# Kernel optimization log

Measured on AMD Instinct MI355X. Metric: run time of the kernel, lower is better.

## Reference

```python
import jax, jax.numpy as jnp
import numpy as np

N, D, K = 131072, 64, 4096


def setup_inputs() -> dict:
    key = jax.random.key(0)
    k1, k2 = jax.random.split(key)
    x = jax.random.normal(k1, (N, D), dtype=jnp.float32)
    embed = jax.random.normal(k2, (K, D), dtype=jnp.float32)
    return {"x": x, "embed": embed}


def reference(x, embed):
    """EuclideanCodebook forward.

    x:     [N, D] flat input vectors
    embed: [K, D] codebook
    Returns (quantize [N,D], embed_ind [N], cluster_size [K], embed_sum [K,D]).
    cluster_size / embed_sum are the one-hot scatter statistics fed to the
    EMA codebook update (embed_onehot.sum(0) and flatten^T @ embed_onehot).
    """
    num_codes = embed.shape[0]
    x2 = jnp.sum(x * x, axis=-1, keepdims=True)               # [N, 1]
    e2 = jnp.sum(embed * embed, axis=-1)                      # [K]
    dist = x2 - 2.0 * (x @ embed.T) + e2[None, :]             # [N, K]
    embed_ind = jnp.argmin(dist, axis=-1)                     # [N]
    quantize = embed[embed_ind]                               # gather [N, D]
    # scatter statistics for EMA update
    cluster_size = jnp.zeros((num_codes,), x.dtype).at[embed_ind].add(1.0)  # [K]
    embed_sum = jax.ops.segment_sum(x, embed_ind, num_segments=num_codes)   # [K, D]
    return quantize, embed_ind, cluster_size, embed_sum
```

## Files before the change

### kernel.cpp

```cpp
#include <hip/hip_runtime.h>

#define N_ROWS 131072
#define DIM 64
#define K_CODES 4096
#define BROWS 128
#define CK 64
#define NCH (K_CODES / CK)
#define EST 72
#define EPS 0.015625f
#define HEPS 0.0078125f

typedef __attribute__((ext_vector_type(8))) short short8;
typedef __attribute__((ext_vector_type(4))) float f32x4;

__device__ inline unsigned short bf16rn(float f) {
    unsigned int u = __float_as_uint(f);
    u += 0x7FFFu + ((u >> 16) & 1u);
    return (unsigned short)(u >> 16);
}
__device__ inline unsigned int fkey(float f) {
    unsigned int u = __float_as_uint(f);
    return (u & 0x80000000u) ? ~u : (u | 0x80000000u);
}

__global__ void pack_kernel(const float* __restrict__ embed,
                            unsigned short* __restrict__ ebf,
                            float* __restrict__ e2,
                            float* __restrict__ e2h,
                            int* __restrict__ cnt,
                            float* __restrict__ cs) {
    const int g = blockIdx.x * blockDim.x + threadIdx.x;
    for (int i = g; i < K_CODES + K_CODES * DIM; i += K_CODES * 16)
        cs[i] = 0.f;
    if (g == 0) *cnt = 0;

    const int code = g >> 4;
    const int w    = g & 15;
    const int half = w >> 3;
    const int d0   = (w & 7) << 3;
    const float* ep = embed + (size_t)code * DIM + d0;
    float4 f0 = *(const float4*)ep;
    float4 f1 = *(const float4*)(ep + 4);
    float wv[8] = {f0.x, f0.y, f0.z, f0.w, f1.x, f1.y, f1.z, f1.w};
    unsigned short o[8];
    float ssq = 0.f;
#pragma unroll
    for (int j = 0; j < 8; ++j) {
        unsigned short hb = bf16rn(wv[j]);
        if (half == 0) {
            o[j] = hb;
            ssq = fmaf(wv[j], wv[j], ssq);
        } else {
            float hf = __uint_as_float(((unsigned int)hb) << 16);
            o[j] = bf16rn(wv[j] - hf);
        }
    }
    *(uint4*)(ebf + (size_t)code * 128 + half * 64 + d0) = *(uint4*)o;
    ssq += __shfl_xor(ssq, 1, 64);
    ssq += __shfl_xor(ssq, 2, 64);
    ssq += __shfl_xor(ssq, 4, 64);
    if (w == 0) {
        e2[code]  = ssq;
        e2h[code] = -0.5f * ssq;
    }
}

__global__ __launch_bounds__(256, 4) void dist_argmin_kernel(
        const float* __restrict__ x, const unsigned short* __restrict__ ebf,
        const float* __restrict__ e2h, const float* __restrict__ embed,
        int* __restrict__ ind_ws, float* __restrict__ ind_out,
        int* __restrict__ cnt, int* __restrict__ list,
        float* __restrict__ quant, float* __restrict__ cs,
        float* __restrict__ esum, int fused) {
    __shared__ unsigned short esh[2][CK * EST];
    __shared__ unsigned short esl[2][CK * EST];
    __shared__ float e2s[2][CK];

    const int tid  = threadIdx.x;
    const int l15  = tid & 15;
    const int quad = (tid >> 4) & 3;
    const int wave = tid >> 6;
    const int r0w  = blockIdx.x * BROWS + wave * 32;

    const int col = tid >> 2;
    const int dq  = (tid & 3) * 16;

    uint4 sh0, sh1, sl0, sl1;
    float se2 = 0.f;
    {
        const unsigned short* pp = ebf + (size_t)col * 128 + dq;
        sh0 = *(const uint4*)pp;
        sh1 = *(const uint4*)(pp + 8);
        sl0 = *(const uint4*)(pp + 64);
        sl1 = *(const uint4*)(pp + 72);
        if (tid < CK) se2 = e2h[tid];
    }

    short8 ah[2][2], al[2][2];
#pragma unroll
    for (int i = 0; i < 2; ++i)
#pragma unroll
        for (int s = 0; s < 2; ++s) {
            const float* xp = x + (size_t)(r0w + 16 * i + l15) * DIM + 32 * s + 8 * quad;
            float4 f0 = *(const float4*)xp;
            float4 f1 = *(const float4*)(xp + 4);
            float w[8] = {f0.x, f0.y, f0.z, f0.w, f1.x, f1.y, f1.z, f1.w};
            short8 h, l;
#pragma unroll
            for (int j = 0; j < 8; ++j) {
                unsigned short hb = bf16rn(w[j]);
                float hf = __uint_as_float(((unsigned int)hb) << 16);
                h[j] = (short)hb;
                l[j] = (short)bf16rn(w[j] - hf);
            }
            ah[i][s] = h;
            al[i][s] = l;
        }

    *(uint4*)(&esh[0][col * EST + dq])     = sh0;
    *(uint4*)(&esh[0][col * EST + dq + 8]) = sh1;
    *(uint4*)(&esl[0][col * EST + dq])     = sl0;
    *(uint4*)(&esl[0][col * EST + dq + 8]) = sl1;
    if (tid < CK) e2s[0][tid] = se2;

    float s1[8], s2[8];
    int c1[8];
#pragma unroll
    for (int t = 0; t < 8; ++t) { s1[t] = -3.4e38f; s2[t] = -3.4e38f; c1[t] = 0; }

    __syncthreads();

    int cur = 0;
    for (int ch = 0; ch < NCH; ++ch) {
        {
            const int c0n = ((ch + 1) & (NCH - 1)) * CK;
            const unsigned short* pp = ebf + (size_t)(c0n + col) * 128 + dq;
            sh0 = *(const uint4*)pp;
            sh1 = *(const uint4*)(pp + 8);
            sl0 = *(const uint4*)(pp + 64);
            sl1 = *(const uint4*)(pp + 72);
            if (tid < CK) se2 = e2h[c0n + tid];
        }

        const int c0 = ch * CK;

        f32x4 acc[2][4];
#pragma unroll
        for (int j = 0; j < 4; ++j) {
            const float ev = e2s[cur][16 * j + l15];
            const f32x4 iv = {ev, ev, ev, ev};
            acc[0][j] = iv;
            acc[1][j] = iv;
        }

#pragma unroll
        for (int j = 0; j < 4; ++j) {
            const int cb = (16 * j + l15) * EST + 8 * quad;
            short8 bh0 = *(const short8*)(&esh[cur][cb]);
            short8 bh1 = *(const short8*)(&esh[cur][cb + 32]);
            short8 bl0 = *(const short8*)(&esl[cur][cb]);
            short8 bl1 = *(const short8*)(&esl[cur][cb + 32]);
#pragma unroll
            for (int i = 0; i < 2; ++i) {
                f32x4 a = acc[i][j];
                a = __builtin_amdgcn_mfma_f32_16x16x32_bf16(ah[i][0], bh0, a, 0, 0, 0);
                a = __builtin_amdgcn_mfma_f32_16x16x32_bf16(ah[i][1], bh1, a, 0, 0, 0);
                a = __builtin_amdgcn_mfma_f32_16x16x32_bf16(ah[i][0], bl0, a, 0, 0, 0);
                a = __builtin_amdgcn_mfma_f32_16x16x32_bf16(ah[i][1], bl1, a, 0, 0, 0);
                a = __builtin_amdgcn_mfma_f32_16x16x32_bf16(al[i][0], bh0, a, 0, 0, 0);
                a = __builtin_amdgcn_mfma_f32_16x16x32_bf16(al[i][1], bh1, a, 0, 0, 0);
                acc[i][j] = a;
            }
        }

#pragma unroll
        for (int j = 0; j < 4; ++j) {
            const int c = c0 + 16 * j + l15;
#pragma unroll
            for (int i = 0; i < 2; ++i)
#pragma unroll
                for (int r = 0; r < 4; ++r) {
                    float d = acc[i][j][r];
                    const int st = i * 4 + r;
                    bool gt = d > s1[st];
                    s2[st] = fmaxf(fminf(d, s1[st]), s2[st]);
                    c1[st] = gt ? c : c1[st];
                    s1[st] = fmaxf(s1[st], d);
                }
        }

        const int nxt = cur ^ 1;
        *(uint4*)(&esh[nxt][col * EST + dq])     = sh0;
        *(uint4*)(&esh[nxt][col * EST + dq + 8]) = sh1;
        *(uint4*)(&esl[nxt][col * EST + dq])     = sl0;
        *(uint4*)(&esl[nxt][col * EST + dq + 8]) = sl1;
        if (tid < CK) e2s[nxt][tid] = se2;

        __syncthreads();
        cur = nxt;
    }

#pragma unroll
    for (int st = 0; st < 8; ++st) {
#pragma unroll
        for (int m = 1; m < 16; m <<= 1) {
            float os1 = __shfl_xor(s1[st], m, 64);
            float os2 = __shfl_xor(s2[st], m, 64);
            int   oc1 = __shfl_xor(c1[st], m, 64);
            bool take = (os1 > s1[st]) || (os1 == s1[st] && oc1 < c1[st]);
            float loser = take ? s1[st] : os1;
            s2[st] = fmaxf(fmaxf(s2[st], os2), loser);
            if (take) { s1[st] = os1; c1[st] = oc1; }
        }
    }
    if (l15 == 0) {
#pragma unroll
        for (int st = 0; st < 8; ++st) {
            const int i = st >> 2, r = st & 3;
            const int row = r0w + 16 * i + 4 * quad + r;
            ind_ws[row] = c1[st];
            ind_out[row] = (float)c1[st];
            if (s1[st] - s2[st] < HEPS) {
                int p = atomicAdd(cnt, 1);
                list[p] = row;
            }
        }
    }

    if (fused) {
        int* li = (int*)&esh[0][0];
        if (l15 == 0) {
#pragma unroll
            for (int st = 0; st < 8; ++st) {
                const int i = st >> 2, r = st & 3;
                li[(wave << 5) + 16 * i + 4 * quad + r] = c1[st];
            }
        }
        const int lane = tid & 63;
        for (int t = 0; t < 32; ++t) {
            const int k = li[(wave << 5) + t];
            const size_t row = (size_t)(r0w + t);
            quant[row * DIM + lane] = embed[(size_t)k * DIM + lane];
            float xv = x[row * DIM + lane];
            atomicAdd(&esum[(size_t)k * DIM + lane], xv);
            if (lane == 0) atomicAdd(&cs[k], 1.0f);
        }
    }
}

__global__ void refine_kernel(const float* __restrict__ x,
                              const float* __restrict__ embed,
                              const float* __restrict__ e2g,
                              const int* __restrict__ cnt,
                              const int* __restrict__ list,
                              int* __restrict__ ind_ws,
                              float* __restrict__ ind_out,
                              float* __restrict__ quant,
                              float* __restrict__ cs,
                              float* __restrict__ esum, int fused) {
    __shared__ float xr[DIM];
    __shared__ unsigned long long red[256];
    const int tid = threadIdx.x;
    const int n = *cnt;
    for (int f = blockIdx.x; f < n; f += gridDim.x) {
        const int row = list[f];
        __syncthreads();
        if (tid < 16)
            ((float4*)xr)[tid] = ((const float4*)(x + (size_t)row * DIM))[tid];
        __syncthreads();
        unsigned long long best = ~0ull;
        for (int c = tid; c < K_CODES; c += 256) {
            const float4* ep = (const float4*)(embed + (size_t)c * DIM);
            float d0 = 0.f, d1 = 0.f, d2 = 0.f, d3 = 0.f;
#pragma unroll
            for (int q = 0; q < 16; ++q) {
                float4 ev = ep[q];
                d0 = fmaf(xr[4 * q + 0], ev.x, d0);
                d1 = fmaf(xr[4 * q + 1], ev.y, d1);
                d2 = fmaf(xr[4 * q + 2], ev.z, d2);
                d3 = fmaf(xr[4 * q + 3], ev.w, d3);
            }
            float sc = fmaf(-2.f, (d0 + d1) + (d2 + d3), e2g[c]);
            unsigned long long key =
                ((unsigned long long)fkey(sc) << 32) | (unsigned int)c;
            if (key < best) best = key;
        }
        red[tid] = best;
        __syncthreads();
        for (int w = 128; w > 0; w >>= 1) {
            if (tid < w && red[tid + w] < red[tid]) red[tid] = red[tid + w];
            __syncthreads();
        }
        const int k_new = (int)(red[0] & 0xFFFFFFFFull);
        if (fused) {
            const int k_old = ind_ws[row];
            if (k_new != k_old) {
                if (tid < DIM) {
                    float xv = xr[tid];
                    atomicAdd(&esum[(size_t)k_old * DIM + tid], -xv);
                    atomicAdd(&esum[(size_t)k_new * DIM + tid],  xv);
                    quant[(size_t)row * DIM + tid] =
                        embed[(size_t)k_new * DIM + tid];
                }
                if (tid == 0) {
                    atomicAdd(&cs[k_old], -1.f);
                    atomicAdd(&cs[k_new],  1.f);
                    ind_ws[row] = k_new;
                    ind_out[row] = (float)k_new;
                }
            }
        } else if (tid == 0) {
            ind_ws[row] = k_new;
            ind_out[row] = (float)k_new;
        }
    }
}

__global__ void scatter_kernel(const float* __restrict__ x,
                               const float* __restrict__ embed,
                               const int* __restrict__ ind,
                               float* __restrict__ quant,
                               float* __restrict__ cs,
                               float* __restrict__ esum) {
    const int t = blockIdx.x * blockDim.x + threadIdx.x;
    const int row = t >> 6;
    const int d = t & 63;
    const int k = ind[row];
    quant[t] = embed[(size_t)k * DIM + d];
    atomicAdd(&esum[(size_t)k * DIM + d], x[t]);
    if (d == 0) atomicAdd(&cs[k], 1.0f);
}

extern "C" void kernel_launch(void* const* d_in, const int* in_sizes, int n_in,
                              void* d_out, int out_size, void* d_ws, size_t ws_size,
                              hipStream_t stream) {
    const float* x     = (const float*)d_in[0];
    const float* embed = (const float*)d_in[1];

    float* out     = (float*)d_out;
    float* quant   = out;
    float* ind_out = out + (size_t)N_ROWS * DIM;
    float* cs      = ind_out + N_ROWS;
    float* esum    = cs + K_CODES;

    float* e2   = (float*)d_ws;
    int* cnt    = (int*)(e2 + K_CODES);
    int* list   = cnt + 4;
    int* ind_ws = list + N_ROWS;
    float* e2h  = (float*)(ind_ws + N_ROWS);
    unsigned short* ebf_ws = (unsigned short*)(e2h + K_CODES);
    const size_t ws_need =
        (size_t)((char*)(ebf_ws + (size_t)K_CODES * 128) - (char*)d_ws);

    const int fused = (ws_size >= ws_need) ? 1 : 0;
    unsigned short* ebf = fused ? ebf_ws : (unsigned short*)quant;

    pack_kernel<<<(K_CODES * 16) / 256, 256, 0, stream>>>(
        embed, ebf, e2, e2h, cnt, cs);
    dist_argmin_kernel<<<N_ROWS / BROWS, 256, 0, stream>>>(
        x, ebf, e2h, embed, ind_ws, ind_out, cnt, list, quant, cs, esum, fused);
    refine_kernel<<<512, 256, 0, stream>>>(
        x, embed, e2, cnt, list, ind_ws, ind_out, quant, cs, esum, fused);
    if (!fused)
        scatter_kernel<<<(size_t)N_ROWS * DIM / 256, 256, 0, stream>>>(
            x, embed, ind_ws, quant, cs, esum);
}
```

Baseline: 421.2 us.

## Refine one row per wavefront with shuffle argmin instead of block reduction

The refine kernel now handles four flagged rows per block, one per 64-lane wavefront, each lane scanning a strided subset of codes. The argmin reduction uses wavefront shuffles instead of a shared-memory tree with eight block barriers. This removes most synchronisation per row and makes fuller use of each block. In exchange each lane scans 64 codes serially, and the non-fused path now writes the index only when it changed.

```diff
diff --git a/kernel.cpp b/kernel.cpp
--- a/kernel.cpp
+++ b/kernel.cpp
@@ -248,71 +248,73 @@
     }
 }
 
-__global__ void refine_kernel(const float* __restrict__ x,
-                              const float* __restrict__ embed,
-                              const float* __restrict__ e2g,
-                              const int* __restrict__ cnt,
-                              const int* __restrict__ list,
-                              int* __restrict__ ind_ws,
-                              float* __restrict__ ind_out,
-                              float* __restrict__ quant,
-                              float* __restrict__ cs,
-                              float* __restrict__ esum, int fused) {
-    __shared__ float xr[DIM];
-    __shared__ unsigned long long red[256];
-    const int tid = threadIdx.x;
+__global__ __launch_bounds__(256) void refine_kernel(
+        const float* __restrict__ x,
+        const float* __restrict__ embed,
+        const float* __restrict__ e2g,
+        const int* __restrict__ cnt,
+        const int* __restrict__ list,
+        int* __restrict__ ind_ws,
+        float* __restrict__ ind_out,
+        float* __restrict__ quant,
+        float* __restrict__ cs,
+        float* __restrict__ esum, int fused) {
+    __shared__ float xr[4][DIM];
+    const int tid  = threadIdx.x;
+    const int w    = tid >> 6;
+    const int lane = tid & 63;
     const int n = *cnt;
-    for (int f = blockIdx.x; f < n; f += gridDim.x) {
-        const int row = list[f];
-        __syncthreads();
-        if (tid < 16)
-            ((float4*)xr)[tid] = ((const float4*)(x + (size_t)row * DIM))[tid];
+    for (int f0 = blockIdx.x * 4; f0 < n; f0 += gridDim.x * 4) {
+        const int fi  = f0 + w;
+        const bool act = fi < n;
+        const int row = act ? list[fi] : list[n - 1];
+        xr[w][lane] = x[(size_t)row * DIM + lane];
         __syncthreads();
         unsigned long long best = ~0ull;
-        for (int c = tid; c < K_CODES; c += 256) {
+        for (int p = 0; p < K_CODES / 64; ++p) {
+            const int c = (p << 6) + lane;
             const float4* ep = (const float4*)(embed + (size_t)c * DIM);
             float d0 = 0.f, d1 = 0.f, d2 = 0.f, d3 = 0.f;
-#pragma unroll
+#pragma unroll 4
             for (int q = 0; q < 16; ++q) {
                 float4 ev = ep[q];
-                d0 = fmaf(xr[4 * q + 0], ev.x, d0);
-                d1 = fmaf(xr[4 * q + 1], ev.y, d1);
-                d2 = fmaf(xr[4 * q + 2], ev.z, d2);
-                d3 = fmaf(xr[4 * q + 3], ev.w, d3);
+                d0 = fmaf(xr[w][4 * q + 0], ev.x, d0);
+                d1 = fmaf(xr[w][4 * q + 1], ev.y, d1);
+                d2 = fmaf(xr[w][4 * q + 2], ev.z, d2);
+                d3 = fmaf(xr[w][4 * q + 3], ev.w, d3);
             }
             float sc = fmaf(-2.f, (d0 + d1) + (d2 + d3), e2g[c]);
             unsigned long long key =
                 ((unsigned long long)fkey(sc) << 32) | (unsigned int)c;
-            if (key < best) best = key;
-        }
-        red[tid] = best;
-        __syncthreads();
-        for (int w = 128; w > 0; w >>= 1) {
-            if (tid < w && red[tid + w] < red[tid]) red[tid] = red[tid + w];
-            __syncthreads();
-        }
-        const int k_new = (int)(red[0] & 0xFFFFFFFFull);
-        if (fused) {
+            best = key < best ? key : best;
+        }
+#pragma unroll
+        for (int m = 32; m > 0; m >>= 1) {
+            unsigned long long o = __shfl_xor(best, m, 64);
+            best = o < best ? o : best;
+        }
+        if (act) {
+            const int k_new = (int)(best & 0xFFFFFFFFull);
             const int k_old = ind_ws[row];
             if (k_new != k_old) {
-                if (tid < DIM) {
-                    float xv = xr[tid];
-                    atomicAdd(&esum[(size_t)k_old * DIM + tid], -xv);
-                    atomicAdd(&esum[(size_t)k_new * DIM + tid],  xv);
-                    quant[(size_t)row * DIM + tid] =
-                        embed[(size_t)k_new * DIM + tid];
+                if (fused) {
+                    float xv = xr[w][lane];
+                    atomicAdd(&esum[(size_t)k_old * DIM + lane], -xv);
+                    atomicAdd(&esum[(size_t)k_new * DIM + lane],  xv);
+                    quant[(size_t)row * DIM + lane] =
+                        embed[(size_t)k_new * DIM + lane];
+                    if (lane == 0) {
+                        atomicAdd(&cs[k_old], -1.f);
+                        atomicAdd(&cs[k_new],  1.f);
+                    }
                 }
-                if (tid == 0) {
-                    atomicAdd(&cs[k_old], -1.f);
-                    atomicAdd(&cs[k_new],  1.f);
+                if (lane == 0) {
                     ind_ws[row] = k_new;
                     ind_out[row] = (float)k_new;
                 }
             }
-        } else if (tid == 0) {
-            ind_ws[row] = k_new;
-            ind_out[row] = (float)k_new;
-        }
+        }
+        __syncthreads();
     }
 }
 
```

After: 447.9 us. 1.06x slower.
